# Performance work log

Hardware: AMD Instinct MI355X
Metric: run time of the kernel (lower is better)

The kernel has to match this reference:

```python
import jax, jax.numpy as jnp
import numpy as np

N_NODES = 200_000
N_EDGES = 6_400_000
N_GRAPHS = 512


def _graph_conv(x, src, dst, W_rel, b_rel, W_root, n_nodes):
    # PyG GraphConv (aggr='add'): lin_rel(sum_{j->i} x_j) + lin_root(x_i)
    agg = jax.ops.segment_sum(x[src], dst, num_segments=n_nodes)  # [N, in]
    return agg @ W_rel.T + b_rel + x @ W_root.T


def setup_inputs() -> dict:
    key = jax.random.key(0)
    ks = jax.random.split(key, 12)
    x = jax.random.normal(ks[0], (N_NODES, 3), dtype=jnp.float32)
    edge_index = jax.random.randint(ks[1], (2, N_EDGES), 0, N_NODES, dtype=jnp.int64)
    batch = jnp.sort(jax.random.randint(ks[2], (N_NODES,), 0, N_GRAPHS, dtype=jnp.int64))

    def xavier(k, shape):
        fan_out, fan_in = shape
        lim = np.sqrt(6.0 / (fan_in + fan_out)).astype(np.float32)
        return jax.random.uniform(k, shape, jnp.float32, -lim, lim)

    return {
        "x": x, "edge_index": edge_index, "batch": batch,
        "W1_rel": xavier(ks[3], (32, 3)),  "b1": jnp.zeros((32,), jnp.float32), "W1_root": xavier(ks[4], (32, 3)),
        "W2_rel": xavier(ks[5], (16, 32)), "b2": jnp.zeros((16,), jnp.float32), "W2_root": xavier(ks[6], (16, 32)),
        "W3_rel": xavier(ks[7], (8, 16)),  "b3": jnp.zeros((8,), jnp.float32),  "W3_root": xavier(ks[8], (8, 16)),
        "W_lin": xavier(ks[9], (1, 8)),    "b_lin": jnp.zeros((1,), jnp.float32),
    }


def reference(x, edge_index, batch,
              W1_rel, b1, W1_root,
              W2_rel, b2, W2_root,
              W3_rel, b3, W3_root,
              W_lin, b_lin):
    src, dst = edge_index[0], edge_index[1]
    h = jax.nn.relu(_graph_conv(x, src, dst, W1_rel, b1, W1_root, N_NODES))
    h = jax.nn.relu(_graph_conv(h, src, dst, W2_rel, b2, W2_root, N_NODES))
    h = jax.nn.relu(_graph_conv(h, src, dst, W3_rel, b3, W3_root, N_NODES))
    pooled = jax.ops.segment_max(h, batch, num_segments=N_GRAPHS)  # [G, 8]
    out = pooled @ W_lin.T + b_lin  # [G, 1]
    return out[:, 0]
```

## Files before the change

### kernel.cpp

```cpp
#include <hip/hip_runtime.h>
#include <hip/hip_fp16.h>

#define N_NODES 200000
#define N_EDGES 6400000
#define N_GRAPHS 512

#define NB 3125
#define CHUNK 8192
#define NCH 782
#define NGRP 25
#define CPG 32
#define SEG 13
#define SCAP 3072

typedef float vf4 __attribute__((ext_vector_type(4)));
typedef float vf2 __attribute__((ext_vector_type(2)));
typedef unsigned vu2 __attribute__((ext_vector_type(2)));

__device__ __forceinline__ unsigned ntload_u(const unsigned* p) {
  return __builtin_nontemporal_load(p);
}
__device__ __forceinline__ int ntload_i(const int* p) { return __builtin_nontemporal_load(p); }
__device__ __forceinline__ float ntload_f(const float* p) {
  return __builtin_nontemporal_load(p);
}
__device__ __forceinline__ float2 ntload_f2(const float* p) {
  vf2 v = __builtin_nontemporal_load((const vf2*)p);
  return make_float2(v.x, v.y);
}
__device__ __forceinline__ void ntstore_u2(unsigned* p, uint2 v) {
  vu2 t = {v.x, v.y};
  __builtin_nontemporal_store(t, (vu2*)p);
}
__device__ __forceinline__ void ntstore_f2(float* p, float2 v) {
  vf2 t = {v.x, v.y};
  __builtin_nontemporal_store(t, (vf2*)p);
}
__device__ __forceinline__ void ntstore_f4(float* p, float4 v) {
  vf4 t = {v.x, v.y, v.z, v.w};
  __builtin_nontemporal_store(t, (vf4*)p);
}
__device__ __forceinline__ void ntstore_u(unsigned* p, unsigned v) {
  __builtin_nontemporal_store(v, p);
}


__global__ __launch_bounds__(256) void count_kernel(const int* __restrict__ dst,
                                                    unsigned short* __restrict__ H) {
  __shared__ unsigned hist[NB];
  for (int i = threadIdx.x; i < NB; i += 256) hist[i] = 0;
  __syncthreads();
  int c = blockIdx.x;
  long e0 = (long)c * CHUNK;
  long rem = (long)N_EDGES - e0;
  int n = rem > CHUNK ? CHUNK : (int)rem;
  for (int i = threadIdx.x; i < n; i += 256) atomicAdd(&hist[dst[e0 + i] >> 6], 1u);
  __syncthreads();
  for (int i = threadIdx.x; i < NB; i += 256) H[(size_t)c * NB + i] = (unsigned short)hist[i];
}

__global__ __launch_bounds__(256) void scan_bins1_kernel(unsigned short* __restrict__ H,
                                                         unsigned* __restrict__ P) {
  int b = blockIdx.x * 256 + threadIdx.x;
  int g = blockIdx.y;
  if (b >= NB) return;
  int c0 = g * CPG, c1 = min(NCH, (g + 1) * CPG);
  unsigned run = 0;
  for (int c = c0; c < c1; c++) {
    unsigned t = H[(size_t)c * NB + b];
    H[(size_t)c * NB + b] = (unsigned short)run;
    run += t;
  }
  P[(size_t)g * NB + b] = run;
}

__global__ __launch_bounds__(256) void scan_bins2_kernel(unsigned* __restrict__ P,
                                                         unsigned* __restrict__ bucketTotal) {
  int b = blockIdx.x * 256 + threadIdx.x;
  if (b >= NB) return;
  unsigned run = 0;
  for (int g = 0; g < NGRP; g++) {
    unsigned t = P[(size_t)g * NB + b];
    P[(size_t)g * NB + b] = run;
    run += t;
  }
  bucketTotal[b] = run;
}

__global__ __launch_bounds__(256) void scan_total_kernel(const unsigned* __restrict__ bucketTotal,
                                                         unsigned* __restrict__ bucketStart) {
  __shared__ unsigned sv[256 * SEG];
  __shared__ unsigned partial[256];
  int t = threadIdx.x;
  for (int i = t; i < 256 * SEG; i += 256) sv[i] = (i < NB) ? bucketTotal[i] : 0u;
  __syncthreads();
  unsigned sum = 0;
#pragma unroll
  for (int k = 0; k < SEG; k++) sum += sv[t * SEG + k];
  partial[t] = sum;
  __syncthreads();
  for (int off = 1; off < 256; off <<= 1) {
    unsigned add = (t >= off) ? partial[t - off] : 0u;
    __syncthreads();
    partial[t] += add;
    __syncthreads();
  }
  unsigned run = partial[t] - sum;
#pragma unroll
  for (int k = 0; k < SEG; k++) {
    unsigned w = sv[t * SEG + k];
    sv[t * SEG + k] = run;
    run += w;
  }
  __syncthreads();
  for (int i = t; i < NB; i += 256) bucketStart[i] = sv[i];
  if (t == 0) bucketStart[NB] = N_EDGES;
}

__global__ __launch_bounds__(256) void scatter_sorted_kernel(
    const int* __restrict__ src, const int* __restrict__ dst,
    const unsigned short* __restrict__ H, const unsigned* __restrict__ P,
    const unsigned* __restrict__ bucketStart, unsigned* __restrict__ packed) {
  __shared__ unsigned ssort[CHUNK];
  __shared__ unsigned short sbort[CHUNK];
  __shared__ unsigned hist[3328];
  __shared__ unsigned cur[3328];
  __shared__ unsigned partial[256];
  int t = threadIdx.x;
  int c = blockIdx.x;
  int g = c / CPG;
  long e0 = (long)c * CHUNK;
  long rem = (long)N_EDGES - e0;
  int n = rem > CHUNK ? CHUNK : (int)rem;
  for (int i = t; i < 3328; i += 256) hist[i] = 0;
  __syncthreads();
  for (int i = t; i < n; i += 256) atomicAdd(&hist[dst[e0 + i] >> 6], 1u);
  __syncthreads();
  unsigned a[SEG], sum = 0;
#pragma unroll
  for (int k = 0; k < SEG; k++) { a[k] = hist[SEG * t + k]; sum += a[k]; }
  partial[t] = sum;
  __syncthreads();
  for (int off = 1; off < 256; off <<= 1) {
    unsigned add = (t >= off) ? partial[t - off] : 0u;
    __syncthreads();
    partial[t] += add;
    __syncthreads();
  }
  unsigned run = partial[t] - sum;
#pragma unroll
  for (int k = 0; k < SEG; k++) {
    hist[SEG * t + k] = run;
    cur[SEG * t + k] = run;
    run += a[k];
  }
  __syncthreads();
  for (int i = t; i < n; i += 256) {
    int d = dst[e0 + i], s = src[e0 + i];
    int b = d >> 6;
    unsigned r = atomicAdd(&cur[b], 1u);
    ssort[r] = ((unsigned)s << 7) | (unsigned)(d & 63);
    sbort[r] = (unsigned short)b;
  }
  __syncthreads();
  for (int b = t; b < NB; b += 256)
    cur[b] = bucketStart[b] + P[(size_t)g * NB + b] + H[(size_t)c * NB + b] - hist[b];
  __syncthreads();
  for (int j = t; j < n; j += 256) packed[cur[sbort[j]] + j] = ssort[j];
}

__global__ __launch_bounds__(256) void sort2_kernel(const unsigned* __restrict__ packedA,
                                                    const unsigned* __restrict__ bucketStart,
                                                    unsigned* __restrict__ packedB,
                                                    unsigned* __restrict__ nodeStart) {
  __shared__ unsigned buf[SCAP];
  __shared__ unsigned buf2[SCAP];
  __shared__ unsigned hist[64], base[64], cur[64];
  int t = threadIdx.x, b = blockIdx.x;
  unsigned s0 = bucketStart[b], s1 = bucketStart[b + 1];
  int n = (int)(s1 - s0);
  if (t < 64) hist[t] = 0;
  for (int i = t; i < n; i += 256) buf[i] = packedA[s0 + i];
  __syncthreads();
  for (int i = t; i < n; i += 256) atomicAdd(&hist[buf[i] & 63u], 1u);
  __syncthreads();
  if (t == 0) {
    unsigned run = 0;
    for (int k = 0; k < 64; k++) {
      unsigned v = hist[k];
      base[k] = run;
      cur[k] = run;
      run += v;
    }
  }
  __syncthreads();
  if (t < 64) nodeStart[b * 64 + t] = s0 + base[t];
  for (int i = t; i < n; i += 256) {
    unsigned p = buf[i];
    unsigned pos = atomicAdd(&cur[p & 63u], 1u);
    buf2[pos] = p >> 7;
  }
  __syncthreads();
  for (int i = t; i < n; i += 256) packedB[s0 + i] = buf2[i];
  if (b == NB - 1 && t == 0) nodeStart[N_NODES] = N_EDGES;
}

__global__ __launch_bounds__(256) void xpad_kernel(const float* __restrict__ x,
                                                   float4* __restrict__ xp) {
  int n = blockIdx.x * 256 + threadIdx.x;
  if (n >= N_NODES) return;
  xp[n] = make_float4(x[3 * n], x[3 * n + 1], x[3 * n + 2], 0.f);
}

__device__ __forceinline__ void half8_unpack(uint4 g, float* f) {
  const __half2* h2 = reinterpret_cast<const __half2*>(&g);
#pragma unroll
  for (int j = 0; j < 4; j++) {
    float2 fj = __half22float2(h2[j]);
    f[2 * j] = fj.x;
    f[2 * j + 1] = fj.y;
  }
}

__global__ __launch_bounds__(256) void layer1_kernel(
    const unsigned* __restrict__ packed, const unsigned* __restrict__ nodeStart,
    const float4* __restrict__ xp,
    const float* __restrict__ W1_rel, const float* __restrict__ b1,
    const float* __restrict__ W1_root,
    const float* __restrict__ W2_rel, const float* __restrict__ W2_root,
    unsigned* __restrict__ t2h, float* __restrict__ r2) {
  __shared__ float sW1rel[96], sW1root[96], sb1[32], sW2rel[512], sW2root[512];
  __shared__ float plds[256 * 4];
  for (int i = threadIdx.x; i < 96; i += 256) { sW1rel[i] = W1_rel[i]; sW1root[i] = W1_root[i]; }
  for (int i = threadIdx.x; i < 32; i += 256) sb1[i] = b1[i];
  for (int i = threadIdx.x; i < 512; i += 256) { sW2rel[i] = W2_rel[i]; sW2root[i] = W2_root[i]; }
  __syncthreads();
  int t = threadIdx.x, ln = t >> 2, part = t & 3;
  int node = blockIdx.x * 64 + ln;
  unsigned s1v = ntload_u(&nodeStart[node + 1]);
  float a0 = 0.f, a1 = 0.f, a2 = 0.f;
  for (unsigned base = ntload_u(&nodeStart[node]) + part; base < s1v; base += 16) {
    unsigned i1 = base + 4, i2 = base + 8, i3 = base + 12;
    unsigned e0 = ntload_u(&packed[base]);
    unsigned e1 = ntload_u(&packed[i1]);
    unsigned e2 = ntload_u(&packed[i2]);
    unsigned e3 = ntload_u(&packed[i3]);
    float4 g0 = xp[e0], g1 = xp[e1], g2 = xp[e2], g3 = xp[e3];
    float m1 = (i1 < s1v) ? 1.f : 0.f;
    float m2 = (i2 < s1v) ? 1.f : 0.f;
    float m3 = (i3 < s1v) ? 1.f : 0.f;
    a0 += g0.x + m1 * g1.x + m2 * g2.x + m3 * g3.x;
    a1 += g0.y + m1 * g1.y + m2 * g2.y + m3 * g3.y;
    a2 += g0.z + m1 * g1.z + m2 * g2.z + m3 * g3.z;
  }
  plds[t * 4] = a0; plds[t * 4 + 1] = a1; plds[t * 4 + 2] = a2;
  __syncthreads();
  int pb = ln * 16;
  float A0 = plds[pb] + plds[pb + 4] + plds[pb + 8] + plds[pb + 12];
  float A1 = plds[pb + 1] + plds[pb + 5] + plds[pb + 9] + plds[pb + 13];
  float A2 = plds[pb + 2] + plds[pb + 6] + plds[pb + 10] + plds[pb + 14];
  float4 xv = xp[node];
  float h[32];
#pragma unroll
  for (int k = 0; k < 32; k++) {
    float v = sW1rel[3 * k] * A0 + sW1rel[3 * k + 1] * A1 + sW1rel[3 * k + 2] * A2 +
              sW1root[3 * k] * xv.x + sW1root[3 * k + 1] * xv.y + sW1root[3 * k + 2] * xv.z +
              sb1[k];
    h[k] = fmaxf(v, 0.f);
  }
  int jb = part * 4;
  float tv[4], rv[4];
#pragma unroll
  for (int j = 0; j < 4; j++) {
    float acc = 0.f, accr = 0.f;
#pragma unroll
    for (int k = 0; k < 32; k++) {
      acc += sW2rel[32 * (jb + j) + k] * h[k];
      accr += sW2root[32 * (jb + j) + k] * h[k];
    }
    tv[j] = acc;
    rv[j] = accr;
  }
  __half2 p0 = __halves2half2(__float2half_rn(tv[0]), __float2half_rn(tv[1]));
  __half2 p1 = __halves2half2(__float2half_rn(tv[2]), __float2half_rn(tv[3]));
  ntstore_u2(&t2h[(size_t)node * 8 + part * 2], make_uint2(*(unsigned*)&p0, *(unsigned*)&p1));
  ntstore_f4(&r2[(size_t)node * 16 + jb], make_float4(rv[0], rv[1], rv[2], rv[3]));
}

__global__ __launch_bounds__(256) void layer2_kernel(
    const unsigned* __restrict__ packed, const unsigned* __restrict__ nodeStart,
    const uint4* __restrict__ t2h4, const float* __restrict__ r2,
    const float* __restrict__ b2,
    const float* __restrict__ W3_rel, const float* __restrict__ W3_root,
    unsigned* __restrict__ t3h, float* __restrict__ r3) {
  __shared__ float sW3rel[128], sW3root[128], sb2[16];
  __shared__ float plds[256 * 9];
  __shared__ float hlds[32 * 16];
  for (int i = threadIdx.x; i < 128; i += 256) { sW3rel[i] = W3_rel[i]; sW3root[i] = W3_root[i]; }
  if (threadIdx.x < 16) sb2[threadIdx.x] = b2[threadIdx.x];
  __syncthreads();
  int t = threadIdx.x, ln = t >> 3, p = t & 7;
  int node = blockIdx.x * 32 + ln;
  int half = p & 1;
  unsigned s1v = ntload_u(&nodeStart[node + 1]);
  float acc[8];
#pragma unroll
  for (int j = 0; j < 8; j++) acc[j] = 0.f;
  for (unsigned base = ntload_u(&nodeStart[node]) + (p >> 1); base < s1v; base += 16) {
    unsigned i1 = base + 4, i2 = base + 8, i3 = base + 12;
    unsigned e0 = ntload_u(&packed[base]);
    unsigned e1 = ntload_u(&packed[i1]);
    unsigned e2 = ntload_u(&packed[i2]);
    unsigned e3 = ntload_u(&packed[i3]);
    uint4 g0 = t2h4[(size_t)e0 * 2 + half];
    uint4 g1 = t2h4[(size_t)e1 * 2 + half];
    uint4 g2 = t2h4[(size_t)e2 * 2 + half];
    uint4 g3 = t2h4[(size_t)e3 * 2 + half];
    float m1 = (i1 < s1v) ? 1.f : 0.f;
    float m2 = (i2 < s1v) ? 1.f : 0.f;
    float m3 = (i3 < s1v) ? 1.f : 0.f;
    float f0[8], f1[8], f2[8], f3[8];
    half8_unpack(g0, f0);
    half8_unpack(g1, f1);
    half8_unpack(g2, f2);
    half8_unpack(g3, f3);
#pragma unroll
    for (int j = 0; j < 8; j++)
      acc[j] += f0[j] + m1 * f1[j] + m2 * f2[j] + m3 * f3[j];
  }
#pragma unroll
  for (int j = 0; j < 8; j++) plds[t * 9 + j] = acc[j];
  __syncthreads();
  {
    float2 rv = ntload_f2(&r2[(size_t)node * 16 + 2 * p]);
    float hv[2];
#pragma unroll
    for (int k2 = 0; k2 < 2; k2++) {
      int f = 2 * p + k2;
      int fh = f >> 3, fi = f & 7;
      int q0 = (ln * 8 + fh) * 9 + fi;
      float s = plds[q0] + plds[q0 + 18] + plds[q0 + 36] + plds[q0 + 54];
      hv[k2] = s + sb2[f] + (k2 == 0 ? rv.x : rv.y);
    }
    hlds[ln * 16 + 2 * p] = fmaxf(hv[0], 0.f);
    hlds[ln * 16 + 2 * p + 1] = fmaxf(hv[1], 0.f);
  }
  __syncthreads();
  const float* W = (p < 4) ? sW3rel : sW3root;
  int rbase = (p < 4) ? 2 * p : 2 * (p - 4);
  float o0 = 0.f, o1 = 0.f;
#pragma unroll
  for (int k = 0; k < 16; k++) {
    float hv = hlds[ln * 16 + k];
    o0 += W[16 * rbase + k] * hv;
    o1 += W[16 * (rbase + 1) + k] * hv;
  }
  if (p < 4) {
    __half2 pk = __halves2half2(__float2half_rn(o0), __float2half_rn(o1));
    ntstore_u(&t3h[(size_t)node * 4 + p], *(unsigned*)&pk);
  } else {
    ntstore_f2(&r3[(size_t)node * 8 + rbase], make_float2(o0, o1));
  }
}

__global__ __launch_bounds__(256) void layer3_kernel(
    const unsigned* __restrict__ packed, const unsigned* __restrict__ nodeStart,
    const uint4* __restrict__ t3h4, const float* __restrict__ r3,
    const float* __restrict__ b3,
    const int* __restrict__ batch, unsigned* __restrict__ pooled) {
  __shared__ float plds[256 * 9];
  __shared__ float sb3[8];
  if (threadIdx.x < 8) sb3[threadIdx.x] = b3[threadIdx.x];
  __syncthreads();
  int t = threadIdx.x, ln = t >> 3, p = t & 7;
  int node = blockIdx.x * 32 + ln;
  unsigned s1v = ntload_u(&nodeStart[node + 1]);
  float acc[8];
#pragma unroll
  for (int j = 0; j < 8; j++) acc[j] = 0.f;
  for (unsigned base = ntload_u(&nodeStart[node]) + p; base < s1v; base += 32) {
    unsigned i1 = base + 8, i2 = base + 16, i3 = base + 24;
    unsigned e0 = ntload_u(&packed[base]);
    unsigned e1 = ntload_u(&packed[i1]);
    unsigned e2 = ntload_u(&packed[i2]);
    unsigned e3 = ntload_u(&packed[i3]);
    uint4 g0 = t3h4[e0];
    uint4 g1 = t3h4[e1];
    uint4 g2 = t3h4[e2];
    uint4 g3 = t3h4[e3];
    float m1 = (i1 < s1v) ? 1.f : 0.f;
    float m2 = (i2 < s1v) ? 1.f : 0.f;
    float m3 = (i3 < s1v) ? 1.f : 0.f;
    float f0[8], f1[8], f2[8], f3[8];
    half8_unpack(g0, f0);
    half8_unpack(g1, f1);
    half8_unpack(g2, f2);
    half8_unpack(g3, f3);
#pragma unroll
    for (int j = 0; j < 8; j++)
      acc[j] += f0[j] + m1 * f1[j] + m2 * f2[j] + m3 * f3[j];
  }
#pragma unroll
  for (int j = 0; j < 8; j++) plds[t * 9 + j] = acc[j];
  __syncthreads();
  int gg = ntload_i(&batch[node]);
  int q0 = ln * 72 + p;
  float v = plds[q0] + plds[q0 + 9] + plds[q0 + 18] + plds[q0 + 27] +
            plds[q0 + 36] + plds[q0 + 45] + plds[q0 + 54] + plds[q0 + 63];
  float h = fmaxf(v + sb3[p] + ntload_f(&r3[(size_t)node * 8 + p]), 0.f);
  atomicMax(&pooled[8 * gg + p], __float_as_uint(h));
}

__global__ __launch_bounds__(256) void final_kernel(
    const unsigned* __restrict__ pooled, const float* __restrict__ W_lin,
    const float* __restrict__ b_lin, float* __restrict__ out) {
  int g = blockIdx.x * blockDim.x + threadIdx.x;
  if (g >= N_GRAPHS) return;
  float acc = b_lin[0];
#pragma unroll
  for (int f = 0; f < 8; f++) acc += __uint_as_float(pooled[8 * g + f]) * W_lin[f];
  out[g] = acc;
}

extern "C" void kernel_launch(void* const* d_in, const int* in_sizes, int n_in,
                              void* d_out, int out_size, void* d_ws, size_t ws_size,
                              hipStream_t stream) {
  const float* x = (const float*)d_in[0];
  const int* ei = (const int*)d_in[1];
  const int* src = ei;
  const int* dst = ei + N_EDGES;
  const int* batch = (const int*)d_in[2];
  const float* W1_rel = (const float*)d_in[3];
  const float* b1 = (const float*)d_in[4];
  const float* W1_root = (const float*)d_in[5];
  const float* W2_rel = (const float*)d_in[6];
  const float* b2 = (const float*)d_in[7];
  const float* W2_root = (const float*)d_in[8];
  const float* W3_rel = (const float*)d_in[9];
  const float* b3 = (const float*)d_in[10];
  const float* W3_root = (const float*)d_in[11];
  const float* W_lin = (const float*)d_in[12];
  const float* b_lin = (const float*)d_in[13];
  float* out = (float*)d_out;

  char* ws = (char*)d_ws;
  unsigned* packedA = (unsigned*)(ws + 0);
  float* r2 = (float*)(ws + 0);
  float* r3 = (float*)(ws + 12800000);
  unsigned* t3h = (unsigned*)(ws + 19200000);
  float4* xpad = (float4*)(ws + 22400000);
  unsigned short* H = (unsigned short*)(ws + 25600000);
  unsigned* packedB = (unsigned*)(ws + 25600000);
  unsigned* t2h = (unsigned*)(ws + 51200128);
  unsigned* pooled = (unsigned*)(ws + 57600128);
  unsigned* bucketStart = (unsigned*)(ws + 57616512);
  unsigned* bucketTotal = (unsigned*)(ws + 57629016);
  unsigned* P = (unsigned*)(ws + 57641516);
  unsigned* nodeStart = (unsigned*)(ws + 57954016);

  hipMemsetAsync(pooled, 0, N_GRAPHS * 8 * sizeof(unsigned), stream);
  hipMemsetAsync(packedB + N_EDGES, 0, 128, stream);

  count_kernel<<<NCH, 256, 0, stream>>>(dst, H);
  scan_bins1_kernel<<<dim3((NB + 255) / 256, NGRP), 256, 0, stream>>>(H, P);
  scan_bins2_kernel<<<(NB + 255) / 256, 256, 0, stream>>>(P, bucketTotal);
  scan_total_kernel<<<1, 256, 0, stream>>>(bucketTotal, bucketStart);
  scatter_sorted_kernel<<<NCH, 256, 0, stream>>>(src, dst, H, P, bucketStart, packedA);
  sort2_kernel<<<NB, 256, 0, stream>>>(packedA, bucketStart, packedB, nodeStart);
  xpad_kernel<<<(N_NODES + 255) / 256, 256, 0, stream>>>(x, xpad);

  layer1_kernel<<<NB, 256, 0, stream>>>(packedB, nodeStart, xpad,
                                        W1_rel, b1, W1_root, W2_rel, W2_root, t2h, r2);
  layer2_kernel<<<N_NODES / 32, 256, 0, stream>>>(packedB, nodeStart, (const uint4*)t2h, r2, b2,
                                                  W3_rel, W3_root, t3h, r3);
  layer3_kernel<<<N_NODES / 32, 256, 0, stream>>>(packedB, nodeStart, (const uint4*)t3h, r3, b3,
                                                  batch, pooled);
  final_kernel<<<(N_GRAPHS + 255) / 256, 256, 0, stream>>>(pooled, W_lin, b_lin, out);
}
```

Measured before the change: 501.1 us.

## Replace count-and-scan bucketing with atomic reservation into padded buckets

Drops the separate count kernel and the multi-level per-chunk histogram scans. Each scatter block now reserves space per bucket with a global atomicAdd and writes into fixed-capacity padded bucket slots, so the edge array is read once instead of twice. A small scan over bucket totals still builds bucketStart for the second-level sort. The cost is a fixed bucket capacity of 2560, which would overflow if a bucket held more edges than that (expected about 2048 for random inputs), and edge order inside each bucket is no longer deterministic.

```diff
diff --git a/kernel.cpp b/kernel.cpp
--- a/kernel.cpp
+++ b/kernel.cpp
@@ -8,10 +8,9 @@
 #define NB 3125
 #define CHUNK 8192
 #define NCH 782
-#define NGRP 25
-#define CPG 32
 #define SEG 13
-#define SCAP 3072
+#define SCAP_PAD 2560
+#define SCAP 2560
 
 typedef float vf4 __attribute__((ext_vector_type(4)));
 typedef float vf2 __attribute__((ext_vector_type(2)));
@@ -44,83 +43,9 @@
   __builtin_nontemporal_store(v, p);
 }
 
-
-__global__ __launch_bounds__(256) void count_kernel(const int* __restrict__ dst,
-                                                    unsigned short* __restrict__ H) {
-  __shared__ unsigned hist[NB];
-  for (int i = threadIdx.x; i < NB; i += 256) hist[i] = 0;
-  __syncthreads();
-  int c = blockIdx.x;
-  long e0 = (long)c * CHUNK;
-  long rem = (long)N_EDGES - e0;
-  int n = rem > CHUNK ? CHUNK : (int)rem;
-  for (int i = threadIdx.x; i < n; i += 256) atomicAdd(&hist[dst[e0 + i] >> 6], 1u);
-  __syncthreads();
-  for (int i = threadIdx.x; i < NB; i += 256) H[(size_t)c * NB + i] = (unsigned short)hist[i];
-}
-
-__global__ __launch_bounds__(256) void scan_bins1_kernel(unsigned short* __restrict__ H,
-                                                         unsigned* __restrict__ P) {
-  int b = blockIdx.x * 256 + threadIdx.x;
-  int g = blockIdx.y;
-  if (b >= NB) return;
-  int c0 = g * CPG, c1 = min(NCH, (g + 1) * CPG);
-  unsigned run = 0;
-  for (int c = c0; c < c1; c++) {
-    unsigned t = H[(size_t)c * NB + b];
-    H[(size_t)c * NB + b] = (unsigned short)run;
-    run += t;
-  }
-  P[(size_t)g * NB + b] = run;
-}
-
-__global__ __launch_bounds__(256) void scan_bins2_kernel(unsigned* __restrict__ P,
-                                                         unsigned* __restrict__ bucketTotal) {
-  int b = blockIdx.x * 256 + threadIdx.x;
-  if (b >= NB) return;
-  unsigned run = 0;
-  for (int g = 0; g < NGRP; g++) {
-    unsigned t = P[(size_t)g * NB + b];
-    P[(size_t)g * NB + b] = run;
-    run += t;
-  }
-  bucketTotal[b] = run;
-}
-
-__global__ __launch_bounds__(256) void scan_total_kernel(const unsigned* __restrict__ bucketTotal,
-                                                         unsigned* __restrict__ bucketStart) {
-  __shared__ unsigned sv[256 * SEG];
-  __shared__ unsigned partial[256];
-  int t = threadIdx.x;
-  for (int i = t; i < 256 * SEG; i += 256) sv[i] = (i < NB) ? bucketTotal[i] : 0u;
-  __syncthreads();
-  unsigned sum = 0;
-#pragma unroll
-  for (int k = 0; k < SEG; k++) sum += sv[t * SEG + k];
-  partial[t] = sum;
-  __syncthreads();
-  for (int off = 1; off < 256; off <<= 1) {
-    unsigned add = (t >= off) ? partial[t - off] : 0u;
-    __syncthreads();
-    partial[t] += add;
-    __syncthreads();
-  }
-  unsigned run = partial[t] - sum;
-#pragma unroll
-  for (int k = 0; k < SEG; k++) {
-    unsigned w = sv[t * SEG + k];
-    sv[t * SEG + k] = run;
-    run += w;
-  }
-  __syncthreads();
-  for (int i = t; i < NB; i += 256) bucketStart[i] = sv[i];
-  if (t == 0) bucketStart[NB] = N_EDGES;
-}
-
-__global__ __launch_bounds__(256) void scatter_sorted_kernel(
+__global__ __launch_bounds__(256) void scatter_reserve_kernel(
     const int* __restrict__ src, const int* __restrict__ dst,
-    const unsigned short* __restrict__ H, const unsigned* __restrict__ P,
-    const unsigned* __restrict__ bucketStart, unsigned* __restrict__ packed) {
+    unsigned* __restrict__ bucketCur, unsigned* __restrict__ packedPad) {
   __shared__ unsigned ssort[CHUNK];
   __shared__ unsigned short sbort[CHUNK];
   __shared__ unsigned hist[3328];
@@ -128,7 +53,6 @@
   __shared__ unsigned partial[256];
   int t = threadIdx.x;
   int c = blockIdx.x;
-  int g = c / CPG;
   long e0 = (long)c * CHUNK;
   long rem = (long)N_EDGES - e0;
   int n = rem > CHUNK ? CHUNK : (int)rem;
@@ -163,13 +87,49 @@
     sbort[r] = (unsigned short)b;
   }
   __syncthreads();
-  for (int b = t; b < NB; b += 256)
-    cur[b] = bucketStart[b] + P[(size_t)g * NB + b] + H[(size_t)c * NB + b] - hist[b];
-  __syncthreads();
-  for (int j = t; j < n; j += 256) packed[cur[sbort[j]] + j] = ssort[j];
-}
-
-__global__ __launch_bounds__(256) void sort2_kernel(const unsigned* __restrict__ packedA,
+#pragma unroll
+  for (int k = 0; k < SEG; k++) {
+    int b = SEG * t + k;
+    if (b < NB && a[k] > 0) {
+      unsigned base = atomicAdd(&bucketCur[b], a[k]);
+      cur[b] = (unsigned)b * SCAP_PAD + base - hist[b];
+    }
+  }
+  __syncthreads();
+  for (int j = t; j < n; j += 256) packedPad[cur[sbort[j]] + j] = ssort[j];
+}
+
+__global__ __launch_bounds__(256) void scan_total_kernel(const unsigned* __restrict__ bucketCur,
+                                                         unsigned* __restrict__ bucketStart) {
+  __shared__ unsigned sv[256 * SEG];
+  __shared__ unsigned partial[256];
+  int t = threadIdx.x;
+  for (int i = t; i < 256 * SEG; i += 256) sv[i] = (i < NB) ? bucketCur[i] : 0u;
+  __syncthreads();
+  unsigned sum = 0;
+#pragma unroll
+  for (int k = 0; k < SEG; k++) sum += sv[t * SEG + k];
+  partial[t] = sum;
+  __syncthreads();
+  for (int off = 1; off < 256; off <<= 1) {
+    unsigned add = (t >= off) ? partial[t - off] : 0u;
+    __syncthreads();
+    partial[t] += add;
+    __syncthreads();
+  }
+  unsigned run = partial[t] - sum;
+#pragma unroll
+  for (int k = 0; k < SEG; k++) {
+    unsigned w = sv[t * SEG + k];
+    sv[t * SEG + k] = run;
+    run += w;
+  }
+  __syncthreads();
+  for (int i = t; i < NB; i += 256) bucketStart[i] = sv[i];
+  if (t == 0) bucketStart[NB] = N_EDGES;
+}
+
+__global__ __launch_bounds__(256) void sort2_kernel(const unsigned* __restrict__ packedPad,
                                                     const unsigned* __restrict__ bucketStart,
                                                     unsigned* __restrict__ packedB,
                                                     unsigned* __restrict__ nodeStart) {
@@ -179,8 +139,9 @@
   int t = threadIdx.x, b = blockIdx.x;
   unsigned s0 = bucketStart[b], s1 = bucketStart[b + 1];
   int n = (int)(s1 - s0);
+  size_t pbase = (size_t)b * SCAP_PAD;
   if (t < 64) hist[t] = 0;
-  for (int i = t; i < n; i += 256) buf[i] = packedA[s0 + i];
+  for (int i = t; i < n; i += 256) buf[i] = packedPad[pbase + i];
   __syncthreads();
   for (int i = t; i < n; i += 256) atomicAdd(&hist[buf[i] & 63u], 1u);
   __syncthreads();
@@ -444,29 +405,25 @@
   float* out = (float*)d_out;
 
   char* ws = (char*)d_ws;
-  unsigned* packedA = (unsigned*)(ws + 0);
-  float* r2 = (float*)(ws + 0);
-  float* r3 = (float*)(ws + 12800000);
-  unsigned* t3h = (unsigned*)(ws + 19200000);
-  float4* xpad = (float4*)(ws + 22400000);
-  unsigned short* H = (unsigned short*)(ws + 25600000);
-  unsigned* packedB = (unsigned*)(ws + 25600000);
+  unsigned* packedB = (unsigned*)(ws + 0);
+  unsigned* packedPad = (unsigned*)(ws + 25600128);
+  float* r2 = (float*)(ws + 25600128);
+  float* r3 = (float*)(ws + 38400128);
+  unsigned* t3h = (unsigned*)(ws + 44800128);
+  float4* xpad = (float4*)(ws + 48000128);
   unsigned* t2h = (unsigned*)(ws + 51200128);
   unsigned* pooled = (unsigned*)(ws + 57600128);
   unsigned* bucketStart = (unsigned*)(ws + 57616512);
-  unsigned* bucketTotal = (unsigned*)(ws + 57629016);
-  unsigned* P = (unsigned*)(ws + 57641516);
-  unsigned* nodeStart = (unsigned*)(ws + 57954016);
+  unsigned* bucketCur = (unsigned*)(ws + 57629016);
+  unsigned* nodeStart = (unsigned*)(ws + 57641516);
 
   hipMemsetAsync(pooled, 0, N_GRAPHS * 8 * sizeof(unsigned), stream);
+  hipMemsetAsync(bucketCur, 0, NB * sizeof(unsigned), stream);
   hipMemsetAsync(packedB + N_EDGES, 0, 128, stream);
 
-  count_kernel<<<NCH, 256, 0, stream>>>(dst, H);
-  scan_bins1_kernel<<<dim3((NB + 255) / 256, NGRP), 256, 0, stream>>>(H, P);
-  scan_bins2_kernel<<<(NB + 255) / 256, 256, 0, stream>>>(P, bucketTotal);
-  scan_total_kernel<<<1, 256, 0, stream>>>(bucketTotal, bucketStart);
-  scatter_sorted_kernel<<<NCH, 256, 0, stream>>>(src, dst, H, P, bucketStart, packedA);
-  sort2_kernel<<<NB, 256, 0, stream>>>(packedA, bucketStart, packedB, nodeStart);
+  scatter_reserve_kernel<<<NCH, 256, 0, stream>>>(src, dst, bucketCur, packedPad);
+  scan_total_kernel<<<1, 256, 0, stream>>>(bucketCur, bucketStart);
+  sort2_kernel<<<NB, 256, 0, stream>>>(packedPad, bucketStart, packedB, nodeStart);
   xpad_kernel<<<(N_NODES + 255) / 256, 256, 0, stream>>>(x, xpad);
 
   layer1_kernel<<<NB, 256, 0, stream>>>(packedB, nodeStart, xpad,
```

Result: slower. 640.8 us (+27.9%).
